# Optimization experiments

Hardware: AMD Instinct MI355X
Metric: run time of the kernel (lower is better)

## Reference

```python
import jax, jax.numpy as jnp
import numpy as np
from jax import lax

KS = 3       # kernel_size
PAD = 1      # padding
STRIDE = 1
DIL = 2      # dilation (scales adaptive offsets)
N = KS * KS
DN = ('NCHW', 'OIHW', 'NCHW')


def _conv(x, w, stride, padding):
    return lax.conv_general_dilated(x, w, (stride, stride),
                                    [(padding, padding), (padding, padding)],
                                    dimension_numbers=DN)


def _deform_forward(x, w_p, b_p, w_m, w_ad, w_conv):
    B, C, H, W = x.shape
    offset = _conv(x, w_p, STRIDE, 1) + b_p[None, :, None, None]      # (B,2N,H,W)
    ad_base = 1.0 - jax.nn.sigmoid(_conv(x, w_ad, STRIDE, 1))         # (B,KS,H,W)
    ad = jnp.tile(ad_base, (1, 2 * KS, 1, 1)) * DIL                   # (B,2N,H,W)
    ad_m = jnp.tile((ad_base - 0.5) * 2.0, (1, KS, 1, 1)) * DIL       # (B,N,H,W)
    m = jax.nn.sigmoid(_conv(x, w_m, STRIDE, 1))                      # (B,N,H,W)

    # kernel relative offsets p_n: (1,2N,1,1)
    r = jnp.arange(-(KS - 1) // 2, (KS - 1) // 2 + 1, dtype=x.dtype)
    pnx, pny = jnp.meshgrid(r, r, indexing='ij')
    p_n = jnp.concatenate([pnx.ravel(), pny.ravel()])[None, :, None, None]
    # base sampling coords p_0: (1,2N,H,W), offset by 1 to match zero padding
    ix = jnp.arange(1, H * STRIDE + 1, STRIDE, dtype=x.dtype)
    iy = jnp.arange(1, W * STRIDE + 1, STRIDE, dtype=x.dtype)
    p0x, p0y = jnp.meshgrid(ix, iy, indexing='ij')
    p_0 = jnp.concatenate([jnp.broadcast_to(p0x, (1, N, H, W)),
                           jnp.broadcast_to(p0y, (1, N, H, W))], axis=1)

    p = p_0 + p_n + offset + ad * p_n                                  # (B,2N,H,W)
    p = p.transpose(0, 2, 3, 1)                                        # (B,H,W,2N)

    xp = jnp.pad(x, ((0, 0), (0, 0), (PAD, PAD), (PAD, PAD)))         # (B,C,Hp,Wp)
    Hp, Wp = H + 2 * PAD, W + 2 * PAD

    q_lt = jnp.floor(p)
    q_rb = q_lt + 1.0

    def clampxy(q):
        return jnp.concatenate([jnp.clip(q[..., :N], 0, Hp - 1),
                                jnp.clip(q[..., N:], 0, Wp - 1)], -1).astype(jnp.int32)

    q_lt = clampxy(q_lt)
    q_rb = clampxy(q_rb)
    q_lb = jnp.concatenate([q_lt[..., :N], q_rb[..., N:]], -1)
    q_rt = jnp.concatenate([q_rb[..., :N], q_lt[..., N:]], -1)

    # out-of-range mask (detached); snap those points to floor, then clamp
    mask = jnp.concatenate([
        (p[..., :N] < PAD) | (p[..., :N] > Hp - 1 - PAD),
        (p[..., N:] < PAD) | (p[..., N:] > Wp - 1 - PAD)], -1).astype(p.dtype)
    mask = lax.stop_gradient(mask)
    p = p * (1 - mask) + jnp.floor(p) * mask
    p = jnp.concatenate([jnp.clip(p[..., :N], 0, Hp - 1),
                         jnp.clip(p[..., N:], 0, Wp - 1)], -1)

    def g(q, sx, sy):  # bilinear weights
        qx = q[..., :N].astype(p.dtype)
        qy = q[..., N:].astype(p.dtype)
        return (1 + sx * (qx - p[..., :N])) * (1 + sy * (qy - p[..., N:]))

    g_lt = g(q_lt, 1, 1)
    g_rb = g(q_rb, -1, -1)
    g_lb = g(q_lb, 1, -1)
    g_rt = g(q_rt, -1, 1)

    x_flat = xp.reshape(B, C, Hp * Wp)
    L = H * W * N

    def gather(q):
        idx = (q[..., :N] * Wp + q[..., N:]).reshape(B, 1, L)
        idx = jnp.broadcast_to(idx, (B, C, L))
        return jnp.take_along_axis(x_flat, idx, axis=2).reshape(B, C, H, W, N)

    x_off = (g_lt[:, None] * gather(q_lt) + g_rb[:, None] * gather(q_rb)
             + g_lb[:, None] * gather(q_lb) + g_rt[:, None] * gather(q_rt))

    # modulation scaled by adaptive term
    mm = (m * ad_m).transpose(0, 2, 3, 1)[:, None]                     # (B,1,H,W,N)
    x_off = x_off * mm

    # (B,C,H,W,ks*ks) -> (B,C,H*ks,W*ks)
    x_off = x_off.reshape(B, C, H, W, KS, KS).transpose(0, 1, 2, 4, 3, 5)
    x_off = x_off.reshape(B, C, H * KS, W * KS)
    return _conv(x_off, w_conv, KS, 0)                                 # (B,Cout,H,W)


def setup_inputs() -> dict:
    key = jax.random.key(0)
    ks = jax.random.split(key, 6)
    C_in, C_out = 64, 64
    x = jax.random.normal(ks[0], (2, C_in, 128, 128), jnp.float32)
    w_p = jax.random.normal(ks[1], (2 * N, C_in, 3, 3), jnp.float32) * 0.01
    b_p = jax.random.normal(ks[2], (2 * N,), jnp.float32) * 0.01
    w_m = jax.random.normal(ks[3], (N, C_in, 3, 3), jnp.float32) * 0.05
    w_ad = jax.random.normal(ks[4], (KS, C_in, 3, 3), jnp.float32) * 0.05
    w_conv = jax.random.normal(ks[5], (C_out, C_in, KS, KS), jnp.float32) / np.sqrt(C_in * N).astype(np.float32)
    return {"x": x, "w_p": w_p, "b_p": b_p, "w_m": w_m, "w_ad": w_ad, "w_conv": w_conv}


def reference(x, w_p, b_p, w_m, w_ad, w_conv):
    return _deform_forward(x, w_p, b_p, w_m, w_ad, w_conv)
```

## Files before the change

### kernel.cpp

```cpp
#include <hip/hip_runtime.h>
#include <hip/hip_fp16.h>
#include <math.h>

#define H 128
#define W 128
#define BATCH 2

typedef short short8 __attribute__((ext_vector_type(8)));
typedef float f32x4 __attribute__((ext_vector_type(4)));
typedef float f32x16 __attribute__((ext_vector_type(16)));

#define BPLANE 1081600
#define PLANE  2163200
#define XS_M   PLANE
#define WC_OFF (2 * PLANE)
#define WM_OFF (WC_OFF + 36864)
#define WM_PLANE 18432
#define META_OFF (WM_OFF + 2 * WM_PLANE)

__device__ __forceinline__ unsigned f2bf_u(float f) {
    union { float f; unsigned u; } v; v.f = f;
    return (v.u + 0x7FFFu + ((v.u >> 16) & 1u)) >> 16;
}
__device__ __forceinline__ float bfbits2f(unsigned lo16) {
    union { unsigned u; float f; } v; v.u = lo16 << 16;
    return v.f;
}
__device__ __forceinline__ float bfs2f(short s) {
    union { unsigned u; float f; } v; v.u = ((unsigned)(unsigned short)s) << 16;
    return v.f;
}
__device__ __forceinline__ void split2(float v, unsigned& h, unsigned& m) {
    h = f2bf_u(v);
    float r1 = v - bfbits2f(h);
    m = f2bf_u(r1);
}

__global__ __launch_bounds__(512) void prep_kernel(
    const float* __restrict__ x, const float* __restrict__ w_p,
    const float* __restrict__ w_m, const float* __restrict__ w_ad,
    const float* __restrict__ w_conv, unsigned short* __restrict__ ws)
{
    const int blk = blockIdx.x, t = threadIdx.x;
    if (blk < 264) {
        int xcd = blk & 7, q = blk >> 3;
        int sub = xcd & 3, b = xcd >> 2;
        int hrow;
        if (sub == 0)      { if (q > 32) return; hrow = q; }
        else if (sub == 3) { if (q > 32) return; hrow = 97 + q; }
        else               { if (q > 31) return; hrow = sub * 32 + 1 + q; }
        size_t rb = ((size_t)b * 16900 + hrow * 130) * 32;
        unsigned* uh = (unsigned*)ws + rb;
        unsigned* um = (unsigned*)(ws + XS_M) + rb;
        if (hrow == 0 || hrow == 129) {
            for (int f = t; f < 4160; f += 512) { uh[f] = 0; um[f] = 0; }
            return;
        }
        __shared__ float s[64 * 129];
        int h = hrow - 1;
        for (int f = t; f < 64 * 32; f += 512) {
            int ci = f >> 5, w4 = f & 31;
            *(float4*)&s[ci * 129 + w4 * 4] =
                *(const float4*)&x[((size_t)(b * 64 + ci) * 128 + h) * 128 + w4 * 4];
        }
        __syncthreads();
        for (int f = t; f < 128 * 8; f += 512) {
            int w = f >> 3, g = f & 7;
            unsigned hv[4], mv[4];
            #pragma unroll
            for (int p = 0; p < 4; ++p) {
                int cip = g * 4 + p;
                unsigned h0, m0, h1, m1;
                split2(s[(2 * cip) * 129 + w], h0, m0);
                split2(s[(2 * cip + 1) * 129 + w], h1, m1);
                hv[p] = h0 | (h1 << 16);
                mv[p] = m0 | (m1 << 16);
            }
            int o = (w + 1) * 32 + g * 4;
            *(uint4*)&uh[o] = make_uint4(hv[0], hv[1], hv[2], hv[3]);
            *(uint4*)&um[o] = make_uint4(mv[0], mv[1], mv[2], mv[3]);
        }
        if (t < 32)      { uh[t] = 0; um[t] = 0; }
        else if (t < 64) { int o = 129 * 32 + (t - 32); uh[o] = 0; um[o] = 0; }
    } else if (blk < 282) {
        int q = (blk - 264) * 512 + t;
        int e = q * 4;
        int j = e & 15, co = (e >> 4) & 63, kk = e >> 10;
        int klin = kk * 16 + j;
        int n = klin >> 6, ci = klin & 63;
        const float* src = w_conv + co * 576 + n;
        ushort4 r;
        r.x = (unsigned short)f2bf_u(src[(ci + 0) * 9]);
        r.y = (unsigned short)f2bf_u(src[(ci + 1) * 9]);
        r.z = (unsigned short)f2bf_u(src[(ci + 2) * 9]);
        r.w = (unsigned short)f2bf_u(src[(ci + 3) * 9]);
        *(ushort4*)(ws + WC_OFF + e) = r;
    } else {
        int q = (blk - 282) * 512 + t;
        int oc = (q >> 4) & 31, j = q & 15, kk = q >> 9;
        int klin = kk * 16 + j;
        int s = klin >> 6, ci = klin & 63;
        float v = 0.f;
        if (oc < 18)      v = w_p[oc * 576 + ci * 9 + s];
        else if (oc < 21) v = w_ad[(oc - 18) * 576 + ci * 9 + s];
        else if (oc < 30) v = w_m[(oc - 21) * 576 + ci * 9 + s];
        unsigned hh, mm; split2(v, hh, mm);
        ws[WM_OFF + q] = (unsigned short)hh;
        ws[WM_OFF + WM_PLANE + q] = (unsigned short)mm;
    }
}

__global__ __launch_bounds__(512, 2) void meta_kernel(
    const float* __restrict__ b_p, const unsigned short* __restrict__ wsu,
    float* __restrict__ meta)
{
    __shared__ __align__(16) float s_part[8 * 16 * 65];
    const int t = threadIdx.x;
    const int d = blockIdx.x;
    const int l = (d & 7) * 32 + (d >> 3);
    const int b = l >> 7, i = l & 127;
    const unsigned short* xsb = wsu + (size_t)b * BPLANE;

    const int w = t >> 6, lane = t & 63;
    const int colA = lane & 31, hi = lane >> 5;
    const int pt = w >> 1, kh = w & 1;
    const int px = pt * 32 + colA;

    f32x16 accA = {0,0,0,0,0,0,0,0,0,0,0,0,0,0,0,0};
    f32x16 accB = {0,0,0,0,0,0,0,0,0,0,0,0,0,0,0,0};
    #pragma unroll
    for (int it = 0; it < 18; ++it) {
        int kk = kh * 18 + it;
        int s = kk >> 2;
        int sr = s / 3, sc = s - sr * 3;
        const unsigned short* bp = xsb + ((i + sr) * 130 + (px + sc)) * 64
                                   + (kk & 3) * 16 + hi * 8;
        const unsigned short* ap = wsu + WM_OFF + (kk * 32 + colA) * 16 + hi * 8;
        short8 ah = *(const short8*)ap;
        short8 am = *(const short8*)(ap + WM_PLANE);
        short8 bh = *(const short8*)bp;
        short8 bm = *(const short8*)(bp + XS_M);
        accA = __builtin_amdgcn_mfma_f32_32x32x16_bf16(ah, bh, accA, 0, 0, 0);
        accB = __builtin_amdgcn_mfma_f32_32x32x16_bf16(am, bh, accB, 0, 0, 0);
        accB = __builtin_amdgcn_mfma_f32_32x32x16_bf16(ah, bm, accB, 0, 0, 0);
    }
    #pragma unroll
    for (int r = 0; r < 16; ++r)
        s_part[(w * 16 + r) * 65 + lane] = accA[r] + accB[r];
    __syncthreads();

    for (int o = t; o < 4096; o += 512) {
        int oc = o & 31, px2 = o >> 5;
        if (oc < 30) {
            int pt2 = px2 >> 5, col = px2 & 31;
            int lane2 = col + ((oc >> 2) & 1) * 32;
            int reg = (oc & 3) + 4 * (oc >> 3);
            float v = s_part[((pt2 * 2 + 0) * 16 + reg) * 65 + lane2]
                    + s_part[((pt2 * 2 + 1) * 16 + reg) * 65 + lane2];
            if (oc < 18)      v += b_p[oc];
            else if (oc < 21) v = 1.f - 1.f / (1.f + expf(-v));
            else              v = 1.f / (1.f + expf(-v));
            meta[(((size_t)b * 128 + i) * 128 + px2) * 32 + oc] = v;
        }
    }
}

__global__ __launch_bounds__(512, 8) void deform_kernel(
    const unsigned short* __restrict__ wsu, const float* __restrict__ meta,
    float* __restrict__ out)
{
    __shared__ __align__(16) char smem[40832];
    unsigned short* s_valb = (unsigned short*)smem;
    __half2* s_gh = (__half2*)(smem + 37376);
    int* s_idxp = (int*)(smem + 39680);

    const int t = threadIdx.x;
    const int d = blockIdx.x;
    const int l = (d & 7) * 128 + (d >> 3);
    const int jb = l & 3, i = (l >> 2) & 127, b = l >> 9;
    const int j0 = jb * 32;

    if (t < 288) {
        int pix = t / 9, n = t % 9;
        int ki = n / 3, kj = n % 3;
        const float* mrow = meta + (((size_t)b * 128 + i) * 128 + j0 + pix) * 32;
        float adb  = mrow[18 + kj];
        float offx = mrow[n];
        float offy = mrow[9 + n];
        float msig = mrow[21 + n];
        float pnx = (float)(ki - 1), pny = (float)(kj - 1);
        float pxc = (float)(i + 1)        + pnx + offx + 2.f * adb * pnx;
        float pyc = (float)(j0 + pix + 1) + pny + offy + 2.f * adb * pny;

        float flx = floorf(pxc), fly = floorf(pyc);
        int ix0 = (int)fminf(fmaxf(flx,       0.f), 129.f);
        int ix1 = (int)fminf(fmaxf(flx + 1.f, 0.f), 129.f);
        int iy0 = (int)fminf(fmaxf(fly,       0.f), 129.f);
        int iy1 = (int)fminf(fmaxf(fly + 1.f, 0.f), 129.f);

        float ptx = (pxc < 1.f || pxc > 128.f) ? flx : pxc;
        float pty = (pyc < 1.f || pyc > 128.f) ? fly : pyc;
        ptx = fminf(fmaxf(ptx, 0.f), 129.f);
        pty = fminf(fmaxf(pty, 0.f), 129.f);

        float wxl = 1.f + (float)ix0 - ptx;
        float wxr = 1.f - ((float)ix1 - ptx);
        float wyl = 1.f + (float)iy0 - pty;
        float wyr = 1.f - ((float)iy1 - pty);

        float mm = msig * (adb - 0.5f) * 4.f;

        s_gh[t * 2 + 0] = __floats2half2_rn(wxl * wyl * mm, wxr * wyr * mm);
        s_gh[t * 2 + 1] = __floats2half2_rn(wxl * wyr * mm, wxr * wyl * mm);
        s_idxp[t] = ix0 | (ix1 << 8) | (iy0 << 16) | (iy1 << 24);
    }
    __syncthreads();

    const unsigned short* xsb = wsu + (size_t)b * BPLANE;
    #define GATHER(TASK) do {                                                     \
        int task = (TASK);                                                        \
        int n = task >> 8, pix = (task >> 3) & 31, cig = task & 7;                \
        int pk = s_idxp[pix * 9 + n];                                             \
        int ix0 = pk & 255, ix1 = (pk >> 8) & 255;                                \
        int iy0 = (pk >> 16) & 255, iy1 = (pk >> 24) & 255;                       \
        const unsigned short* base = xsb + cig * 8;                               \
        short8 v00 = *(const short8*)(base + (ix0 * 130 + iy0) * 64);             \
        short8 v11 = *(const short8*)(base + (ix1 * 130 + iy1) * 64);             \
        short8 v01 = *(const short8*)(base + (ix0 * 130 + iy1) * 64);             \
        short8 v10 = *(const short8*)(base + (ix1 * 130 + iy0) * 64);             \
        float2 g01 = __half22float2(s_gh[(pix * 9 + n) * 2 + 0]);                 \
        float2 g23 = __half22float2(s_gh[(pix * 9 + n) * 2 + 1]);                 \
        unsigned po[4];                                                           \
        _Pragma("unroll")                                                         \
        for (int jp = 0; jp < 4; ++jp) {                                          \
            float e0 = g01.x * bfs2f(v00[2 * jp])     + g01.y * bfs2f(v11[2 * jp])\
                     + g23.x * bfs2f(v01[2 * jp])     + g23.y * bfs2f(v10[2 * jp]);\
            float e1 = g01.x * bfs2f(v00[2 * jp + 1]) + g01.y * bfs2f(v11[2 * jp + 1])\
                     + g23.x * bfs2f(v01[2 * jp + 1]) + g23.y * bfs2f(v10[2 * jp + 1]);\
            po[jp] = f2bf_u(e0) | (f2bf_u(e1) << 16);                             \
        }                                                                         \
        *(uint4*)(s_valb + pix * 584 + n * 64 + cig * 8)                          \
            = make_uint4(po[0], po[1], po[2], po[3]);                             \
    } while (0)

    #pragma unroll
    for (int it = 0; it < 4; ++it) GATHER(t + it * 512);
    if (t < 256) GATHER(t + 2048);
    #undef GATHER
    __syncthreads();

    {
        const int w = t >> 6, lane = t & 63;
        const int ch = w & 1, kq = w >> 1;
        const int colA = lane & 31, hi = lane >> 5;
        const unsigned short* wa = wsu + WC_OFF + ((kq * 9) * 64 + ch * 32 + colA) * 16 + hi * 8;
        const unsigned short* vb = s_valb + colA * 584 + (kq * 9) * 16 + hi * 8;
        f32x16 acc = {0,0,0,0,0,0,0,0,0,0,0,0,0,0,0,0};
        #pragma unroll
        for (int s = 0; s < 9; ++s) {
            short8 a   = *(const short8*)(wa + s * 1024);
            short8 bfr = *(const short8*)(vb + s * 16);
            acc = __builtin_amdgcn_mfma_f32_32x32x16_bf16(a, bfr, acc, 0, 0, 0);
        }
        __syncthreads();
        float* sp = (float*)smem;
        #pragma unroll
        for (int r = 0; r < 16; ++r)
            sp[(w * 16 + r) * 65 + lane] = acc[r];
        __syncthreads();
        int ch2 = t >> 8, e = t & 255;
        int lane2 = e & 63, rq = e >> 6;
        #pragma unroll
        for (int q = 0; q < 4; ++q) {
            int reg = rq * 4 + q;
            float v = sp[((0 + ch2) * 16 + reg) * 65 + lane2]
                    + sp[((2 + ch2) * 16 + reg) * 65 + lane2]
                    + sp[((4 + ch2) * 16 + reg) * 65 + lane2]
                    + sp[((6 + ch2) * 16 + reg) * 65 + lane2];
            int col = lane2 & 31;
            int row = (reg & 3) + 8 * (reg >> 2) + 4 * (lane2 >> 5);
            int co = ch2 * 32 + row;
            out[(((size_t)b * 64 + co) * 128 + i) * 128 + j0 + col] = v;
        }
    }
}

extern "C" void kernel_launch(void* const* d_in, const int* in_sizes, int n_in,
                              void* d_out, int out_size, void* d_ws, size_t ws_size,
                              hipStream_t stream) {
    const float* x      = (const float*)d_in[0];
    const float* w_p    = (const float*)d_in[1];
    const float* b_p    = (const float*)d_in[2];
    const float* w_m    = (const float*)d_in[3];
    const float* w_ad   = (const float*)d_in[4];
    const float* w_conv = (const float*)d_in[5];
    float* outp = (float*)d_out;
    unsigned short* ws = (unsigned short*)d_ws;
    float* meta_f = (float*)(ws + META_OFF);

    prep_kernel<<<318, 512, 0, stream>>>(x, w_p, w_m, w_ad, w_conv, ws);
    meta_kernel<<<256, 512, 0, stream>>>(b_p, ws, meta_f);
    deform_kernel<<<1024, 512, 0, stream>>>(ws, meta_f, outp);
}
```

Before: 38.67 us.

## Split prep rows into column halves and meta into per-quarter 256-thread blocks

The prep kernel now splits each padded row into two column halves, doubling its block count and halving shared memory per block. The meta kernel moves from 256 blocks of 512 threads to 1024 blocks of 256 threads. Each block covers a 32-pixel quarter of a row, and its four waves split the K dimension nine steps each, with a four-way reduction in LDS. The aim is to raise parallelism and occupancy across the CUs of the two small kernels. The cost is more blocks and some redundant work per block.

```diff
diff --git a/kernel.cpp b/kernel.cpp
--- a/kernel.cpp
+++ b/kernel.cpp
@@ -42,8 +42,9 @@
     const float* __restrict__ w_conv, unsigned short* __restrict__ ws)
 {
     const int blk = blockIdx.x, t = threadIdx.x;
-    if (blk < 264) {
-        int xcd = blk & 7, q = blk >> 3;
+    if (blk < 528) {
+        int xcd = blk & 7, rest = blk >> 3;
+        int chalf = rest & 1, q = rest >> 1;
         int sub = xcd & 3, b = xcd >> 2;
         int hrow;
         if (sub == 0)      { if (q > 32) return; hrow = q; }
@@ -53,37 +54,40 @@
         unsigned* uh = (unsigned*)ws + rb;
         unsigned* um = (unsigned*)(ws + XS_M) + rb;
         if (hrow == 0 || hrow == 129) {
-            for (int f = t; f < 4160; f += 512) { uh[f] = 0; um[f] = 0; }
+            for (int f = t + chalf * 2080; f < 2080 + chalf * 2080; f += 512) {
+                uh[f] = 0; um[f] = 0;
+            }
             return;
         }
-        __shared__ float s[64 * 129];
+        __shared__ float s[64 * 65];
         int h = hrow - 1;
-        for (int f = t; f < 64 * 32; f += 512) {
-            int ci = f >> 5, w4 = f & 31;
-            *(float4*)&s[ci * 129 + w4 * 4] =
-                *(const float4*)&x[((size_t)(b * 64 + ci) * 128 + h) * 128 + w4 * 4];
+        for (int f = t; f < 64 * 16; f += 512) {
+            int ci = f >> 4, w4 = f & 15;
+            *(float4*)&s[ci * 65 + w4 * 4] =
+                *(const float4*)&x[((size_t)(b * 64 + ci) * 128 + h) * 128 + chalf * 64 + w4 * 4];
         }
         __syncthreads();
-        for (int f = t; f < 128 * 8; f += 512) {
+        {
+            int f = t;
             int w = f >> 3, g = f & 7;
             unsigned hv[4], mv[4];
             #pragma unroll
             for (int p = 0; p < 4; ++p) {
                 int cip = g * 4 + p;
                 unsigned h0, m0, h1, m1;
-                split2(s[(2 * cip) * 129 + w], h0, m0);
-                split2(s[(2 * cip + 1) * 129 + w], h1, m1);
+                split2(s[(2 * cip) * 65 + w], h0, m0);
+                split2(s[(2 * cip + 1) * 65 + w], h1, m1);
                 hv[p] = h0 | (h1 << 16);
                 mv[p] = m0 | (m1 << 16);
             }
-            int o = (w + 1) * 32 + g * 4;
+            int o = (chalf * 64 + w + 1) * 32 + g * 4;
             *(uint4*)&uh[o] = make_uint4(hv[0], hv[1], hv[2], hv[3]);
             *(uint4*)&um[o] = make_uint4(mv[0], mv[1], mv[2], mv[3]);
         }
-        if (t < 32)      { uh[t] = 0; um[t] = 0; }
-        else if (t < 64) { int o = 129 * 32 + (t - 32); uh[o] = 0; um[o] = 0; }
-    } else if (blk < 282) {
-        int q = (blk - 264) * 512 + t;
+        if (chalf == 0) { if (t < 32) { uh[t] = 0; um[t] = 0; } }
+        else           { if (t < 32) { int o = 129 * 32 + t; uh[o] = 0; um[o] = 0; } }
+    } else if (blk < 546) {
+        int q = (blk - 528) * 512 + t;
         int e = q * 4;
         int j = e & 15, co = (e >> 4) & 63, kk = e >> 10;
         int klin = kk * 16 + j;
@@ -96,7 +100,7 @@
         r.w = (unsigned short)f2bf_u(src[(ci + 3) * 9]);
         *(ushort4*)(ws + WC_OFF + e) = r;
     } else {
-        int q = (blk - 282) * 512 + t;
+        int q = (blk - 546) * 512 + t;
         int oc = (q >> 4) & 31, j = q & 15, kk = q >> 9;
         int klin = kk * 16 + j;
         int s = klin >> 6, ci = klin & 63;
@@ -110,27 +114,29 @@
     }
 }
 
-__global__ __launch_bounds__(512, 2) void meta_kernel(
+__global__ __launch_bounds__(256, 4) void meta_kernel(
     const float* __restrict__ b_p, const unsigned short* __restrict__ wsu,
     float* __restrict__ meta)
 {
-    __shared__ __align__(16) float s_part[8 * 16 * 65];
+    __shared__ __align__(16) float s_part[4 * 16 * 65];
     const int t = threadIdx.x;
     const int d = blockIdx.x;
-    const int l = (d & 7) * 32 + (d >> 3);
+    const int rest = d >> 3;
+    const int l = (d & 7) * 32 + (rest >> 2);
+    const int quarter = rest & 3;
     const int b = l >> 7, i = l & 127;
+    const int px0 = quarter * 32;
     const unsigned short* xsb = wsu + (size_t)b * BPLANE;
 
     const int w = t >> 6, lane = t & 63;
     const int colA = lane & 31, hi = lane >> 5;
-    const int pt = w >> 1, kh = w & 1;
-    const int px = pt * 32 + colA;
+    const int px = px0 + colA;
 
     f32x16 accA = {0,0,0,0,0,0,0,0,0,0,0,0,0,0,0,0};
     f32x16 accB = {0,0,0,0,0,0,0,0,0,0,0,0,0,0,0,0};
     #pragma unroll
-    for (int it = 0; it < 18; ++it) {
-        int kk = kh * 18 + it;
+    for (int it = 0; it < 9; ++it) {
+        int kk = w * 9 + it;
         int s = kk >> 2;
         int sr = s / 3, sc = s - sr * 3;
         const unsigned short* bp = xsb + ((i + sr) * 130 + (px + sc)) * 64
@@ -149,19 +155,18 @@
         s_part[(w * 16 + r) * 65 + lane] = accA[r] + accB[r];
     __syncthreads();
 
-    for (int o = t; o < 4096; o += 512) {
-        int oc = o & 31, px2 = o >> 5;
-        if (oc < 30) {
-            int pt2 = px2 >> 5, col = px2 & 31;
-            int lane2 = col + ((oc >> 2) & 1) * 32;
-            int reg = (oc & 3) + 4 * (oc >> 3);
-            float v = s_part[((pt2 * 2 + 0) * 16 + reg) * 65 + lane2]
-                    + s_part[((pt2 * 2 + 1) * 16 + reg) * 65 + lane2];
-            if (oc < 18)      v += b_p[oc];
-            else if (oc < 21) v = 1.f - 1.f / (1.f + expf(-v));
-            else              v = 1.f / (1.f + expf(-v));
-            meta[(((size_t)b * 128 + i) * 128 + px2) * 32 + oc] = v;
-        }
+    for (int o = t; o < 960; o += 256) {
+        int oc = o % 30, col = o / 30;
+        int lane2 = col + ((oc >> 2) & 1) * 32;
+        int reg = (oc & 3) + 4 * (oc >> 3);
+        float v = s_part[(0 * 16 + reg) * 65 + lane2]
+                + s_part[(1 * 16 + reg) * 65 + lane2]
+                + s_part[(2 * 16 + reg) * 65 + lane2]
+                + s_part[(3 * 16 + reg) * 65 + lane2];
+        if (oc < 18)      v += b_p[oc];
+        else if (oc < 21) v = 1.f - 1.f / (1.f + expf(-v));
+        else              v = 1.f / (1.f + expf(-v));
+        meta[(((size_t)b * 128 + i) * 128 + px0 + col) * 32 + oc] = v;
     }
 }
 
@@ -298,7 +303,7 @@
     unsigned short* ws = (unsigned short*)d_ws;
     float* meta_f = (float*)(ws + META_OFF);
 
-    prep_kernel<<<318, 512, 0, stream>>>(x, w_p, w_m, w_ad, w_conv, ws);
-    meta_kernel<<<256, 512, 0, stream>>>(b_p, ws, meta_f);
+    prep_kernel<<<582, 512, 0, stream>>>(x, w_p, w_m, w_ad, w_conv, ws);
+    meta_kernel<<<1024, 256, 0, stream>>>(b_p, ws, meta_f);
     deform_kernel<<<1024, 512, 0, stream>>>(ws, meta_f, outp);
 }
```

New measurement: 37.15 us. 1.04x faster.
